# Kernel tuning notes

Measured on AMD Instinct MI355X. Metric: run time of the kernel, lower is better.

Reference implementation:

```python
import jax, jax.numpy as jnp
import numpy as np

B, T, K, U, C, M, H = 64, 600, 10, 64, 54, 20, 512
OUT = 1 + 6 * M        # 121
IN1 = 3 + C            # 57  -> rnn_cell1 input
IN2 = 3 + C + H        # 569 -> rnn_cell2 input
BIAS = 0.0
EPS = 1e-20


def setup_inputs() -> dict:
    key = jax.random.key(0)
    ks = jax.random.split(key, 20)
    p = lambda k, shape: (jax.random.normal(k, shape, dtype=jnp.float32) * 0.05)
    return {
        "x": jax.random.normal(ks[0], (B, T, 3), dtype=jnp.float32),
        "y": jax.random.uniform(ks[1], (B, T, 3), dtype=jnp.float32),
        "c_vec": jax.random.uniform(ks[2], (B, U, C), dtype=jnp.float32),
        "W_ih1": p(ks[3], (4 * H, IN1)), "W_hh1": p(ks[4], (4 * H, H)),
        "b_ih1": p(ks[5], (4 * H,)),     "b_hh1": p(ks[6], (4 * H,)),
        "W_ih2": p(ks[7], (4 * H, IN2)), "W_hh2": p(ks[8], (4 * H, H)),
        "b_ih2": p(ks[9], (4 * H,)),     "b_hh2": p(ks[10], (4 * H,)),
        "W_k": p(ks[11], (3 * K, H)),    "b_k": p(ks[12], (3 * K,)),
        "W_o": p(ks[13], (OUT, H)),      "b_o": p(ks[14], (OUT,)),
    }


def _lstm_cell(xin, h, c, Wih, Whh, bih, bhh):
    g = xin @ Wih.T + h @ Whh.T + bih + bhh          # [B, 4H]
    i, f, gg, o = jnp.split(g, 4, axis=1)            # PyTorch LSTMCell gate order
    c = jax.nn.sigmoid(f) * c + jax.nn.sigmoid(i) * jnp.tanh(gg)
    h = jax.nn.sigmoid(o) * jnp.tanh(c)
    return h, c


def _forward(x, y, c_vec, W_ih1, W_hh1, b_ih1, b_hh1, W_ih2, W_hh2, b_ih2, b_hh2,
             W_k, b_k, W_o, b_o):
    u = jnp.arange(U, dtype=jnp.float32)[None, None, :]   # [1,1,U]
    zB = jnp.zeros((B, H), dtype=x.dtype)

    def step(carry, xt):
        h1, c1, h2, c2, w, kappa = carry
        h1, c1 = _lstm_cell(jnp.concatenate([xt, w], 1), h1, c1, W_ih1, W_hh1, b_ih1, b_hh1)
        kg = h1 @ W_k.T + b_k                               # [B, 3K]
        a_hat, be_hat, ka_hat = jnp.split(kg, 3, axis=1)
        alpha = jnp.exp(a_hat)[:, :, None]                  # [B,K,1]
        beta = jnp.exp(be_hat)[:, :, None]
        kappa = kappa + jnp.exp(ka_hat)[:, :, None]
        phi = jnp.sum(jnp.exp(-beta * (kappa - u) ** 2) * alpha, axis=1)  # [B,U]
        w = jnp.einsum('bu,buc->bc', phi, c_vec)            # [B,C]
        h2, c2 = _lstm_cell(jnp.concatenate([xt, h1, w], 1), h2, c2, W_ih2, W_hh2, b_ih2, b_hh2)
        return (h1, c1, h2, c2, w, kappa), h2

    init = (zB, zB, zB, zB, jnp.zeros((B, C), x.dtype), jnp.zeros((B, K, 1), x.dtype))
    _, h2_seq = jax.lax.scan(step, init, jnp.transpose(x, (1, 0, 2)))   # [T,B,H]
    h2_seq = jnp.transpose(h2_seq, (1, 0, 2)).reshape(-1, H)            # [B*T,H]
    outputs = h2_seq @ W_o.T + b_o                                      # [B*T,OUT]

    y1, y2, s = jnp.moveaxis(y.reshape(-1, 3), 1, 0)                    # each [B*T]
    e = jax.nn.sigmoid(-outputs[:, 0])                                  # 1/(1+exp(o0))
    pi_hat, mu1, mu2, s1_hat, s2_hat, rho_hat = jnp.split(outputs[:, 1:], 6, axis=1)
    pi = jax.nn.softmax(pi_hat, axis=1)
    sigma1 = jnp.exp(s1_hat - BIAS)
    sigma2 = jnp.exp(s2_hat - BIAS)
    rho = jnp.tanh(rho_hat)
    d1 = (y1[:, None] - mu1) / sigma1
    d2 = (y2[:, None] - mu2) / sigma2
    z = d1 ** 2 + d2 ** 2 - 2.0 * rho * d1 * d2
    one_m_r2 = 1.0 - rho ** 2
    gauss = jnp.exp(-z / (2.0 * one_m_r2)) / (2.0 * np.pi * sigma1 * sigma2 * jnp.sqrt(one_m_r2))
    loss_g = jnp.sum(-jnp.log(jnp.sum(pi * gauss, axis=1) + EPS))
    loss_b = jnp.sum(-jnp.log((e + EPS) * s + (1.0 - e + EPS) * (1.0 - s)))
    return (loss_g + loss_b) / (B * T)


def reference(x, y, c_vec, W_ih1, W_hh1, b_ih1, b_hh1, W_ih2, W_hh2, b_ih2, b_hh2,
              W_k, b_k, W_o, b_o):
    return _forward(x, y, c_vec, W_ih1, W_hh1, b_ih1, b_hh1, W_ih2, W_hh2,
                    b_ih2, b_hh2, W_k, b_k, W_o, b_o)
```

## Files before the change

### kernel.cpp

```cpp
#include <hip/hip_runtime.h>
#include <math.h>

typedef _Float16 f16;
typedef _Float16 f16x8 __attribute__((ext_vector_type(8)));
typedef float f32x4 __attribute__((ext_vector_type(4)));
union HU { f16 h; unsigned short u; };

#define NT 512
#define NG1 16
#define G2B 16
#define NG2 16
#define PRB 32
#define ATB 33
#define NBLK 97
#define ABE 69632
#define ABEH 69632
#define OUTG_OFF 69632
#define LOSS_OFF 86016
#define FLAG_OFF 86144
#define W2OFF_F 86400
#define W1OFF_F 1200512
#define WPOFF_F 1790336
#define G2PER 139264
#define G1PER 73728
#define DYN_LDS 136704
#define G1LW 520
#define G2LW 1032
#define PRLW 520

__device__ __forceinline__ f16x8 cld16(const void* p) {
  f16x8 r;
  asm volatile("global_load_dwordx4 %0, %1, off sc0 sc1" : "=v"(r) : "v"(p) : "memory");
  return r;
}
__device__ __forceinline__ unsigned long long ald64(const void* p) {
  return __hip_atomic_load((const unsigned long long*)p, __ATOMIC_RELAXED, __HIP_MEMORY_SCOPE_AGENT);
}
__device__ __forceinline__ unsigned ald32(const void* p) {
  return __hip_atomic_load((const unsigned*)p, __ATOMIC_RELAXED, __HIP_MEMORY_SCOPE_AGENT);
}
__device__ __forceinline__ void cst32(void* p, unsigned v) {
  asm volatile("global_store_dword %0, %1, off sc0 sc1" :: "v"(p), "v"(v) : "memory");
}
__device__ __forceinline__ void cst128h(void* p, f16x8 v) {
  asm volatile("global_store_dwordx4 %0, %1, off sc0 sc1" :: "v"(p), "v"(v) : "memory");
}
__device__ __forceinline__ void cst128f(void* p, f32x4 v) {
  asm volatile("global_store_dwordx4 %0, %1, off sc0 sc1" :: "v"(p), "v"(v) : "memory");
}
#define VMWAIT() do { asm volatile("s_waitcnt vmcnt(0)" ::: "memory"); \
                      __builtin_amdgcn_sched_barrier(0); } while (0)

__device__ __forceinline__ float sigm(float v){ return 1.f/(1.f+expf(-v)); }

__device__ __forceinline__ void gbar(unsigned* flags, unsigned target) {
  VMWAIT();
  __syncthreads();
  if (threadIdx.x == 0) cst32(flags + blockIdx.x, target);
  if (threadIdx.x < 64) {
    bool ok;
    do {
      unsigned lo = target, hi = target;
      if (threadIdx.x < 49) {
        unsigned long long v = ald64(flags + threadIdx.x * 2);
        lo = (unsigned)v; hi = (unsigned)(v >> 32);
      }
      ok = (lo >= target) && (hi >= target);
    } while (!__all(ok));
  }
  __syncthreads();
}

__device__ __forceinline__ void wspin(const unsigned* wflags, unsigned target) {
  int lane = threadIdx.x & 63;
  bool ok;
  do {
    unsigned lo = target, hi = target;
    if (lane < 32) {
      unsigned long long v = ald64(wflags + lane * 2);
      lo = (unsigned)v; hi = (unsigned)(v >> 32);
    }
    ok = (lo >= target) && (hi >= target);
  } while (!__all(ok));
}

__device__ __forceinline__ float mix_loss(const float* so, const float* yl, int t, int m) {
  float y1 = yl[t*3+0], y2 = yl[t*3+1], ys = yl[t*3+2];
  float ph = (m < 20) ? so[1+m] : -1e30f;
  float mx = ph;
  #pragma unroll
  for (int d = 16; d >= 1; d >>= 1) mx = fmaxf(mx, __shfl_xor(mx, d));
  float pe = (m < 20) ? expf(ph - mx) : 0.f;
  float ps = pe;
  #pragma unroll
  for (int d = 16; d >= 1; d >>= 1) ps += __shfl_xor(ps, d);
  float contrib = 0.f;
  if (m < 20) {
    float mu1 = so[21+m], mu2 = so[41+m];
    float s1 = expf(so[61+m]), s2 = expf(so[81+m]);
    float rh = tanhf(so[101+m]);
    float d1 = (y1-mu1)/s1, d2 = (y2-mu2)/s2;
    float omr = 1.f - rh*rh;
    float z = d1*d1 + d2*d2 - 2.f*rh*d1*d2;
    float ga = expf(-z/(2.f*omr)) / (6.283185307179586f * s1 * s2 * sqrtf(omr));
    contrib = (pe/ps)*ga;
  }
  float gs = contrib;
  #pragma unroll
  for (int d = 16; d >= 1; d >>= 1) gs += __shfl_xor(gs, d);
  float lg = -logf(gs + 1e-20f);
  float e = 1.f/(1.f + expf(so[0]));
  float lb = -logf((e + 1e-20f)*ys + (1.f - e + 1e-20f)*(1.f - ys));
  return lg + lb;
}

__global__ __launch_bounds__(256) void k_init(float* ws,
    const float* __restrict__ Wih1, const float* __restrict__ Whh1,
    const float* __restrict__ Wih2, const float* __restrict__ Whh2,
    const float* __restrict__ Wo)
{
  unsigned* w0 = (unsigned*)ws;
  unsigned* fl = (unsigned*)ws + FLAG_OFF;
  int idx = blockIdx.x*256 + threadIdx.x;
  int str = gridDim.x*256;
  for (int e = idx; e < ABE; e += str) w0[e] = 0u;
  for (int e = idx; e < 2*8192 + 64; e += str) w0[OUTG_OFF + e] = 0u;
  if (idx < 256) fl[idx] = (idx < NBLK) ? 0u : (idx < 128 ? 0x7fffffffu : 0u);

  f16* w2p = (f16*)(ws + W2OFF_F);
  f16* w1p = (f16*)(ws + W1OFF_F);
  f16* wpp = (f16*)(ws + WPOFF_F);
  const int G2T = 16*G2PER, G1T = 16*G1PER, PPT = 65536;
  for (int e = idx; e < G2T; e += str) {
    int bi = e / G2PER, r0 = e - bi*G2PER;
    int sub = r0 & 7, frag = r0 >> 3;
    int l = frag & 63, t = frag >> 6;
    int nt = t & 7, j = t >> 3;
    int n = nt*16 + (l & 15);
    int R = (n & 3)*512 + bi*32 + (n >> 2);
    int k = j*32 + ((l >> 4) << 3) + sub;
    float v = 0.f;
    if (k >= 4 && k < 58)        v = Wih2[R*569 + 515 + (k-4)];
    else if (k >= 58 && k < 61)  v = Wih2[R*569 + (k-58)];
    else if (k >= 64 && k < 576) v = Wih2[R*569 + 3 + (k-64)];
    else if (k >= 576)           v = Whh2[R*512 + (k-576)];
    w2p[e] = (f16)v;
  }
  for (int e = idx; e < G1T; e += str) {
    int bi = e / G1PER, r0 = e - bi*G1PER;
    int sub = r0 & 7, frag = r0 >> 3;
    int l = frag & 63, t = frag >> 6;
    int nt = t & 7, j = t >> 3;
    int n = nt*16 + (l & 15);
    int R = (n & 3)*512 + bi*32 + (n >> 2);
    int k = j*32 + ((l >> 4) << 3) + sub;
    float v = 0.f;
    if (k < 3)                   v = Wih1[R*57 + k];
    else if (k >= 4 && k < 58)   v = Wih1[R*57 + 3 + (k-4)];
    else if (k >= 64 && k < 576) v = Whh1[R*512 + (k-64)];
    w1p[e] = (f16)v;
  }
  for (int e = idx; e < PPT; e += str) {
    int sub = e & 7, frag = e >> 3;
    int l = frag & 63, t = frag >> 6;
    int nt = t & 7, j = t >> 3;
    int o = nt*16 + (l & 15);
    int k = j*32 + ((l >> 4) << 3) + sub;
    wpp[e] = (o < 121) ? (f16)Wo[o*512 + k] : (f16)0.f;
  }
}

__global__ __launch_bounds__(NT, 1) void kmain(
    const float* __restrict__ x, const float* __restrict__ y, const float* __restrict__ cvec,
    const float* __restrict__ Wih1, const float* __restrict__ Whh1,
    const float* __restrict__ bih1, const float* __restrict__ bhh1,
    const float* __restrict__ Wih2, const float* __restrict__ Whh2,
    const float* __restrict__ bih2, const float* __restrict__ bhh2,
    const float* __restrict__ Wk, const float* __restrict__ bk,
    const float* __restrict__ Wo, const float* __restrict__ bo,
    float* __restrict__ out, float* __restrict__ ws)
{
  extern __shared__ char dsm[];
  const int blk = blockIdx.x, tid = threadIdx.x;
  const int wv = tid >> 6, l = tid & 63;
  const int q = l & 3;

  f16* AB = (f16*)ws;
  float* outg  = ws + OUTG_OFF;
  float* lossg = ws + LOSS_OFF;
  unsigned* flags  = (unsigned*)ws + FLAG_OFF;
  unsigned* wflags = flags + 128;
  const f16* __restrict__ w2pA = (const f16*)(ws + W2OFF_F);
  const f16* __restrict__ w1pA = (const f16*)(ws + W1OFF_F);
  const f16* __restrict__ wppA = (const f16*)(ws + WPOFF_F);

  f32x4 acc[4];
  float cst[16];
  float bi0 = 0.f, bpr = 0.f, lreg = 0.f;
  #pragma unroll
  for (int z = 0; z < 16; ++z) cst[z] = 0.f;

  if (blk < NG1) {
    int n = wv*16 + (l & 15);
    int R = (n & 3)*512 + blk*32 + (n >> 2);
    bi0 = bih1[R] + bhh1[R];
  } else if (blk < G2B + NG2) {
    const int g2i = blk - G2B;
    int n = wv*16 + (l & 15);
    int R = (n & 3)*512 + g2i*32 + (n >> 2);
    bi0 = bih2[R] + bhh2[R];
  } else if (blk == PRB) {
    int o = wv*16 + (l & 15);
    bpr = (o < 121) ? bo[o] : 0.f;
  } else {
    const int b = blk - ATB;
    f16*   wk  = (f16*)dsm;
    float* cv  = (float*)(dsm + 31200);
    float* xl  = (float*)(dsm + 45024);
    float* yl  = (float*)(dsm + 52224);
    for (int e = tid; e < 30*512; e += NT) { int j = e >> 9, k = e & 511; wk[j*520 + k] = (f16)Wk[e]; }
    for (int e = tid; e < 3456; e += NT) cv[e] = cvec[b*3456 + e];
    for (int e = tid; e < 1800; e += NT) { xl[e] = x[b*1800+e]; yl[e] = y[b*1800+e]; }
    float* kap = (float*)(dsm + 61152);
    if (tid < 10) kap[tid] = 0.f;
    __syncthreads();
    if (tid == 0) {
      HU h0, h1u, h2u;
      h0.h = (f16)xl[0]; h1u.h = (f16)xl[1]; h2u.h = (f16)xl[2];
      cst32((unsigned*)AB + (b*1088 >> 1),       (unsigned)h0.u | ((unsigned)h1u.u << 16));
      cst32((unsigned*)AB + ((b*1088 + 2) >> 1), (unsigned)h2u.u);
    }
  }

  gbar(flags, 1);

  for (int t = 0; t <= 602; ++t) {
    const f16* __restrict__ Acur = AB + (t & 1)*ABEH;
    f16* __restrict__ Anxt = AB + ((t & 1)^1)*ABEH;
    unsigned* AcurW = (unsigned*)Acur;

    if (blk < NG1) {
      if (t <= 599) {
        const f16* __restrict__ wp = w1pA + blk*G1PER;
        f16* plds = (f16*)dsm;
        f16* htr  = (f16*)(dsm + 66560);
        {
          f16x8 tb[8];
          #pragma unroll
          for (int it = 0; it < 8; ++it) {
            int flat = tid + it*512;
            tb[it] = cld16(Acur + (flat >> 6)*1088 + 64 + (flat & 63)*8);
          }
          VMWAIT();
          #pragma unroll
          for (int it = 0; it < 8; ++it) {
            int flat = tid + it*512;
            *(f16x8*)&plds[(flat >> 6)*G1LW + (flat & 63)*8] = tb[it];
          }
        }
        __syncthreads();
        #pragma unroll
        for (int z = 0; z < 4; ++z) acc[z] = (f32x4){0,0,0,0};
        const int kb = (l >> 4)*8;
        #pragma unroll 8
        for (int j = 2; j < 18; ++j) {
          f16x8 bfr = *(const f16x8*)(wp + ((j*8 + wv)*64 + l)*8);
          #pragma unroll
          for (int mt = 0; mt < 4; ++mt) {
            f16x8 af = *(const f16x8*)&plds[((l&15) + 16*mt)*G1LW + (j*32 - 64) + kb];
            acc[mt] = __builtin_amdgcn_mfma_f32_16x16x32_f16(af, bfr, acc[mt], 0,0,0);
          }
        }
        wspin(wflags, (unsigned)t);
        {
          f16x8 a01[4][2];
          #pragma unroll
          for (int mt = 0; mt < 4; ++mt)
            #pragma unroll
            for (int jd = 0; jd < 2; ++jd)
              a01[mt][jd] = cld16(Acur + ((l&15) + 16*mt)*1088 + jd*32 + kb);
          VMWAIT();
          #pragma unroll
          for (int jd = 0; jd < 2; ++jd) {
            f16x8 bfr = *(const f16x8*)(wp + ((jd*8 + wv)*64 + l)*8);
            #pragma unroll
            for (int mt = 0; mt < 4; ++mt)
              acc[mt] = __builtin_amdgcn_mfma_f32_16x16x32_f16(a01[mt][jd], bfr, acc[mt], 0,0,0);
          }
        }
        {
          int dloc = wv*4 + ((l & 15) >> 2);
          #pragma unroll
          for (int mt = 0; mt < 4; ++mt)
            #pragma unroll
            for (int r = 0; r < 4; ++r) {
              float xme = acc[mt][r] + bi0;
              float a1 = __shfl_xor(xme, 1), a2 = __shfl_xor(xme, 2), a3 = __shfl_xor(a1, 2);
              float gi = q==0?xme: q==1?a1 : q==2?a2 : a3;
              float gf = q==0?a1 : q==1?xme: q==2?a3 : a2;
              float gg = q==0?a2 : q==1?a3 : q==2?xme: a1;
              float go = q==0?a3 : q==1?a2 : q==2?a1 : xme;
              float c = cst[mt*4 + r];
              c = sigm(gf)*c + sigm(gi)*tanhf(gg);
              cst[mt*4 + r] = c;
              float h = sigm(go)*tanhf(c);
              if (q == 0) htr[(mt*16 + (l>>4)*4 + r)*32 + dloc] = (f16)h;
            }
        }
        __syncthreads();
        if (tid < 256) {
          int m = tid >> 2, qq = tid & 3;
          f16x8 hv = *(const f16x8*)&htr[m*32 + qq*8];
          cst128h(Anxt + m*1088 + 64 + blk*32 + qq*8, hv);
        }
      }
    } else if (blk < G2B + NG2) {
      if (t >= 1 && t <= 600) {
        const int g2i = blk - G2B;
        const f16* __restrict__ wp = w2pA + g2i*G2PER;
        f16* plds = (f16*)dsm;
        f16* htr  = (f16*)(dsm + 132096);
        {
          f16x8 tb[16];
          #pragma unroll
          for (int it = 0; it < 16; ++it) {
            int flat = tid + it*512;
            tb[it] = cld16(Acur + (flat >> 7)*1088 + 64 + (flat & 127)*8);
          }
          VMWAIT();
          #pragma unroll
          for (int it = 0; it < 16; ++it) {
            int flat = tid + it*512;
            *(f16x8*)&plds[(flat >> 7)*G2LW + (flat & 127)*8] = tb[it];
          }
        }
        __syncthreads();
        #pragma unroll
        for (int z = 0; z < 4; ++z) acc[z] = (f32x4){0,0,0,0};
        const int kb = (l >> 4)*8;
        #pragma unroll 8
        for (int j = 2; j < 34; ++j) {
          f16x8 bfr = *(const f16x8*)(wp + ((j*8 + wv)*64 + l)*8);
          #pragma unroll
          for (int mt = 0; mt < 4; ++mt) {
            f16x8 af = *(const f16x8*)&plds[((l&15) + 16*mt)*G2LW + (j*32 - 64) + kb];
            acc[mt] = __builtin_amdgcn_mfma_f32_16x16x32_f16(af, bfr, acc[mt], 0,0,0);
          }
        }
        wspin(wflags, (unsigned)t);
        {
          f16x8 a01[4][2];
          #pragma unroll
          for (int mt = 0; mt < 4; ++mt)
            #pragma unroll
            for (int jd = 0; jd < 2; ++jd)
              a01[mt][jd] = cld16(Acur + ((l&15) + 16*mt)*1088 + jd*32 + kb);
          VMWAIT();
          #pragma unroll
          for (int jd = 0; jd < 2; ++jd) {
            f16x8 bfr = *(const f16x8*)(wp + ((jd*8 + wv)*64 + l)*8);
            #pragma unroll
            for (int mt = 0; mt < 4; ++mt)
              acc[mt] = __builtin_amdgcn_mfma_f32_16x16x32_f16(a01[mt][jd], bfr, acc[mt], 0,0,0);
          }
        }
        {
          int dloc = wv*4 + ((l & 15) >> 2);
          #pragma unroll
          for (int mt = 0; mt < 4; ++mt)
            #pragma unroll
            for (int r = 0; r < 4; ++r) {
              float xme = acc[mt][r] + bi0;
              float a1 = __shfl_xor(xme, 1), a2 = __shfl_xor(xme, 2), a3 = __shfl_xor(a1, 2);
              float gi = q==0?xme: q==1?a1 : q==2?a2 : a3;
              float gf = q==0?a1 : q==1?xme: q==2?a3 : a2;
              float gg = q==0?a2 : q==1?a3 : q==2?xme: a1;
              float go = q==0?a3 : q==1?a2 : q==2?a1 : xme;
              float c = cst[mt*4 + r];
              c = sigm(gf)*c + sigm(gi)*tanhf(gg);
              cst[mt*4 + r] = c;
              float h = sigm(go)*tanhf(c);
              if (q == 0) htr[(mt*16 + (l>>4)*4 + r)*32 + dloc] = (f16)h;
            }
        }
        __syncthreads();
        if (tid < 256) {
          int m = tid >> 2, qq = tid & 3;
          f16x8 hv = *(const f16x8*)&htr[m*32 + qq*8];
          cst128h(Anxt + m*1088 + 576 + g2i*32 + qq*8, hv);
        }
      }
    } else if (blk == PRB) {
      if (t >= 2 && t <= 601) {
        f16* plds = (f16*)dsm;
        float* otr = (float*)(dsm + 66560);
        float* outp = outg + (t & 1)*8192;
        {
          f16x8 tb[8];
          #pragma unroll
          for (int it = 0; it < 8; ++it) {
            int flat = tid + it*512;
            tb[it] = cld16(Acur + (flat >> 6)*1088 + 576 + (flat & 63)*8);
          }
          VMWAIT();
          #pragma unroll
          for (int it = 0; it < 8; ++it) {
            int flat = tid + it*512;
            *(f16x8*)&plds[(flat >> 6)*PRLW + (flat & 63)*8] = tb[it];
          }
        }
        __syncthreads();
        #pragma unroll
        for (int z = 0; z < 4; ++z) acc[z] = (f32x4){0,0,0,0};
        const int kb = (l >> 4)*8;
        #pragma unroll 8
        for (int j = 0; j < 16; ++j) {
          f16x8 bfr = *(const f16x8*)(wppA + ((j*8 + wv)*64 + l)*8);
          #pragma unroll
          for (int mt = 0; mt < 4; ++mt) {
            f16x8 af = *(const f16x8*)&plds[((l&15) + 16*mt)*PRLW + j*32 + kb];
            acc[mt] = __builtin_amdgcn_mfma_f32_16x16x32_f16(af, bfr, acc[mt], 0,0,0);
          }
        }
        { int o = wv*16 + (l & 15);
          #pragma unroll
          for (int mt = 0; mt < 4; ++mt)
            #pragma unroll
            for (int r = 0; r < 4; ++r)
              otr[(mt*16 + (l>>4)*4 + r)*128 + o] = acc[mt][r] + bpr;
        }
        __syncthreads();
        #pragma unroll
        for (int it = 0; it < 4; ++it) {
          int flat = tid + it*512;
          int m = flat >> 5, o4 = flat & 31;
          f32x4 v4 = *(const f32x4*)&otr[m*128 + o4*4];
          cst128f(outp + m*128 + o4*4, v4);
        }
      }
    } else {
      const int b = blk - ATB;
      f16*   wk   = (f16*)dsm;
      float* cv   = (float*)(dsm + 31200);
      float* xl   = (float*)(dsm + 45024);
      float* yl   = (float*)(dsm + 52224);
      f16*   h1h  = (f16*)(dsm + 59424);
      float* so   = (float*)(dsm + 60448);
      float* skg  = (float*)(dsm + 60944);
      float* sal  = (float*)(dsm + 61072);
      float* sbe  = (float*)(dsm + 61112);
      float* kap  = (float*)(dsm + 61152);
      float* sphi = (float*)(dsm + 61192);
      float* wtmp = (float*)(dsm + 61448);
      if (t >= 1 && t <= 600) {
        const int s = t - 1;
        if (tid < 64) {
          f16x8 hv = cld16(Acur + b*1088 + 64 + tid*8);
          VMWAIT();
          *(f16x8*)&h1h[tid*8] = hv;
        }
        __syncthreads();
        {
          int j = tid >> 4, ksv = tid & 15;
          float a = 0.f;
          if (j < 30) {
            const f16* wr = &wk[j*520 + ksv*32];
            const f16* hr = &h1h[ksv*32];
            #pragma unroll
            for (int c = 0; c < 4; ++c) {
              f16x8 qv = *(const f16x8*)(wr + c*8);
              f16x8 hv = *(const f16x8*)(hr + c*8);
              #pragma unroll
              for (int e = 0; e < 8; ++e) a += (float)qv[e] * (float)hv[e];
            }
          }
          a += __shfl_xor(a, 1); a += __shfl_xor(a, 2);
          a += __shfl_xor(a, 4); a += __shfl_xor(a, 8);
          if (j < 30 && ksv == 0) skg[j] = a + bk[j];
        }
        __syncthreads();
        if (tid < 10) {
          sal[tid] = expf(skg[tid]);
          sbe[tid] = expf(skg[10+tid]);
          kap[tid] += expf(skg[20+tid]);
        }
        __syncthreads();
        if (tid < 64) {
          float u = (float)tid, ph = 0.f;
          #pragma unroll
          for (int k2 = 0; k2 < 10; ++k2) {
            float d = kap[k2] - u;
            ph += sal[k2]*expf(-sbe[k2]*d*d);
          }
          sphi[tid] = ph;
        }
        __syncthreads();
        if (tid < 54) {
          float wvv = 0.f;
          #pragma unroll 8
          for (int u = 0; u < 64; ++u) wvv += sphi[u]*cv[u*54 + tid];
          wtmp[tid] = wvv;
        }
        __syncthreads();
        if (tid < 27) {
          HU a, bu; a.h = (f16)wtmp[2*tid]; bu.h = (f16)wtmp[2*tid+1];
          cst32(AcurW + ((b*1088 + 4 + 2*tid) >> 1), (unsigned)a.u | ((unsigned)bu.u << 16));
        } else if (tid == 27) {
          HU a, bu; a.h = (f16)xl[s*3+0]; bu.h = (f16)xl[s*3+1];
          cst32(AcurW + ((b*1088 + 58) >> 1), (unsigned)a.u | ((unsigned)bu.u << 16));
        } else if (tid == 28) {
          HU a; a.h = (f16)xl[s*3+2];
          cst32(AcurW + ((b*1088 + 60) >> 1), (unsigned)a.u);
        } else if (tid == 29 && s <= 598) {
          HU a, bu; a.h = (f16)xl[(s+1)*3+0]; bu.h = (f16)xl[(s+1)*3+1];
          cst32(AcurW + ((b*1088) >> 1), (unsigned)a.u | ((unsigned)bu.u << 16));
        } else if (tid == 30 && s <= 598) {
          HU a; a.h = (f16)xl[(s+1)*3+2];
          cst32(AcurW + ((b*1088 + 2) >> 1), (unsigned)a.u);
        }
        VMWAIT();
        __syncthreads();
        if (tid == 0) cst32(wflags + b, (unsigned)t);
      }
      if (t >= 3) {
        if (tid < 121) {
          unsigned uu = ald32((unsigned*)(outg + ((t & 1)^1)*8192) + b*128 + tid);
          float v; __builtin_memcpy(&v, &uu, 4);
          so[tid] = v;
        }
        __syncthreads();
        if (tid < 32) {
          float v = mix_loss(so, yl, t-3, tid);
          if (tid == 0) lreg += v;
        }
      }
    }
    gbar(flags, 2 + t);
  }

  if (blk >= ATB && tid == 0) {
    unsigned uu; __builtin_memcpy(&uu, &lreg, 4);
    cst32((unsigned*)lossg + (blk - ATB), uu);
  }
  gbar(flags, 606);
  if (blk == ATB && tid < 64) {
    unsigned uu = ald32((unsigned*)lossg + tid);
    float v; __builtin_memcpy(&v, &uu, 4);
    #pragma unroll
    for (int d = 32; d >= 1; d >>= 1) v += __shfl_xor(v, d);
    if (tid == 0) out[0] = v / 38400.f;
  }
}

extern "C" void kernel_launch(void* const* d_in, const int* in_sizes, int n_in,
                              void* d_out, int out_size, void* d_ws, size_t ws_size,
                              hipStream_t stream)
{
  (void)in_sizes; (void)n_in; (void)out_size; (void)ws_size;
  const float* x    = (const float*)d_in[0];
  const float* y    = (const float*)d_in[1];
  const float* cvec = (const float*)d_in[2];
  const float* Wih1 = (const float*)d_in[3];
  const float* Whh1 = (const float*)d_in[4];
  const float* bih1 = (const float*)d_in[5];
  const float* bhh1 = (const float*)d_in[6];
  const float* Wih2 = (const float*)d_in[7];
  const float* Whh2 = (const float*)d_in[8];
  const float* bih2 = (const float*)d_in[9];
  const float* bhh2 = (const float*)d_in[10];
  const float* Wk   = (const float*)d_in[11];
  const float* bk   = (const float*)d_in[12];
  const float* Wo   = (const float*)d_in[13];
  const float* bo   = (const float*)d_in[14];
  float* out = (float*)d_out;
  float* wsf = (float*)d_ws;

  hipFuncSetAttribute((const void*)kmain, hipFuncAttributeMaxDynamicSharedMemorySize, DYN_LDS);

  k_init<<<256, 256, 0, stream>>>(wsf, Wih1, Whh1, Wih2, Whh2, Wo);

  void* args[] = {
    (void*)&x, (void*)&y, (void*)&cvec,
    (void*)&Wih1, (void*)&Whh1, (void*)&bih1, (void*)&bhh1,
    (void*)&Wih2, (void*)&Whh2, (void*)&bih2, (void*)&bhh2,
    (void*)&Wk, (void*)&bk, (void*)&Wo, (void*)&bo,
    (void*)&out, (void*)&wsf
  };
  hipLaunchCooperativeKernel((void*)kmain, dim3(NBLK), dim3(NT), args, DYN_LDS, stream);
}
```

Before: 12.80 ms.

## Restructure per-step pipeline so attention waits on h1 flags within the step

Attention blocks now compute the window vector for step t in the same global-barrier interval. They spin on new per-block h1 flags written by the LSTM1 blocks, then write w into the next buffer. LSTM1 no longer waits on attention flags mid-GEMM and loads the full input row (x, w and h1) in one pass. Barrier flags are padded to separate 64-byte slots to avoid false sharing during polling. This changes the cross-stage schedule and dependency chain, with some risk of lengthening the critical path within each step.

```diff
diff --git a/kernel.cpp b/kernel.cpp
--- a/kernel.cpp
+++ b/kernel.cpp
@@ -18,13 +18,14 @@
 #define OUTG_OFF 69632
 #define LOSS_OFF 86016
 #define FLAG_OFF 86144
-#define W2OFF_F 86400
-#define W1OFF_F 1200512
-#define WPOFF_F 1790336
+#define HFLG_OFF 87744
+#define W2OFF_F 88064
+#define W1OFF_F 1202176
+#define WPOFF_F 1792000
 #define G2PER 139264
 #define G1PER 73728
 #define DYN_LDS 136704
-#define G1LW 520
+#define G1LW 584
 #define G2LW 1032
 #define PRLW 520
 
@@ -33,9 +34,6 @@
   asm volatile("global_load_dwordx4 %0, %1, off sc0 sc1" : "=v"(r) : "v"(p) : "memory");
   return r;
 }
-__device__ __forceinline__ unsigned long long ald64(const void* p) {
-  return __hip_atomic_load((const unsigned long long*)p, __ATOMIC_RELAXED, __HIP_MEMORY_SCOPE_AGENT);
-}
 __device__ __forceinline__ unsigned ald32(const void* p) {
   return __hip_atomic_load((const unsigned*)p, __ATOMIC_RELAXED, __HIP_MEMORY_SCOPE_AGENT);
 }
@@ -56,32 +54,17 @@
 __device__ __forceinline__ void gbar(unsigned* flags, unsigned target) {
   VMWAIT();
   __syncthreads();
-  if (threadIdx.x == 0) cst32(flags + blockIdx.x, target);
+  if (threadIdx.x == 0) cst32(flags + blockIdx.x * 16, target);
   if (threadIdx.x < 64) {
+    int lane = threadIdx.x;
     bool ok;
     do {
-      unsigned lo = target, hi = target;
-      if (threadIdx.x < 49) {
-        unsigned long long v = ald64(flags + threadIdx.x * 2);
-        lo = (unsigned)v; hi = (unsigned)(v >> 32);
-      }
-      ok = (lo >= target) && (hi >= target);
+      unsigned v0 = ald32(flags + lane * 16);
+      unsigned v1 = (lane < 33) ? ald32(flags + (64 + lane) * 16) : target;
+      ok = (v0 >= target) && (v1 >= target);
     } while (!__all(ok));
   }
   __syncthreads();
-}
-
-__device__ __forceinline__ void wspin(const unsigned* wflags, unsigned target) {
-  int lane = threadIdx.x & 63;
-  bool ok;
-  do {
-    unsigned lo = target, hi = target;
-    if (lane < 32) {
-      unsigned long long v = ald64(wflags + lane * 2);
-      lo = (unsigned)v; hi = (unsigned)(v >> 32);
-    }
-    ok = (lo >= target) && (hi >= target);
-  } while (!__all(ok));
 }
 
 __device__ __forceinline__ float mix_loss(const float* so, const float* yl, int t, int m) {
@@ -120,12 +103,11 @@
     const float* __restrict__ Wo)
 {
   unsigned* w0 = (unsigned*)ws;
-  unsigned* fl = (unsigned*)ws + FLAG_OFF;
   int idx = blockIdx.x*256 + threadIdx.x;
   int str = gridDim.x*256;
   for (int e = idx; e < ABE; e += str) w0[e] = 0u;
   for (int e = idx; e < 2*8192 + 64; e += str) w0[OUTG_OFF + e] = 0u;
-  if (idx < 256) fl[idx] = (idx < NBLK) ? 0u : (idx < 128 ? 0x7fffffffu : 0u);
+  for (int e = idx; e < HFLG_OFF + 256 - FLAG_OFF; e += str) w0[FLAG_OFF + e] = 0u;
 
   f16* w2p = (f16*)(ws + W2OFF_F);
   f16* w1p = (f16*)(ws + W1OFF_F);
@@ -189,7 +171,7 @@
   float* outg  = ws + OUTG_OFF;
   float* lossg = ws + LOSS_OFF;
   unsigned* flags  = (unsigned*)ws + FLAG_OFF;
-  unsigned* wflags = flags + 128;
+  unsigned* hflags = (unsigned*)ws + HFLG_OFF;
   const f16* __restrict__ w2pA = (const f16*)(ws + W2OFF_F);
   const f16* __restrict__ w1pA = (const f16*)(ws + W1OFF_F);
   const f16* __restrict__ wppA = (const f16*)(ws + WPOFF_F);
@@ -237,55 +219,40 @@
   for (int t = 0; t <= 602; ++t) {
     const f16* __restrict__ Acur = AB + (t & 1)*ABEH;
     f16* __restrict__ Anxt = AB + ((t & 1)^1)*ABEH;
-    unsigned* AcurW = (unsigned*)Acur;
+    unsigned* AnxtW = (unsigned*)Anxt;
 
     if (blk < NG1) {
       if (t <= 599) {
         const f16* __restrict__ wp = w1pA + blk*G1PER;
         f16* plds = (f16*)dsm;
-        f16* htr  = (f16*)(dsm + 66560);
-        {
-          f16x8 tb[8];
-          #pragma unroll
-          for (int it = 0; it < 8; ++it) {
-            int flat = tid + it*512;
-            tb[it] = cld16(Acur + (flat >> 6)*1088 + 64 + (flat & 63)*8);
+        f16* htr  = (f16*)(dsm + 74752);
+        {
+          f16x8 tb[9];
+          #pragma unroll
+          for (int it = 0; it < 9; ++it) {
+            int flat = it*512 + tid;
+            int row = flat / 72, c8 = flat - row*72;
+            tb[it] = cld16(Acur + row*1088 + c8*8);
           }
           VMWAIT();
           #pragma unroll
-          for (int it = 0; it < 8; ++it) {
-            int flat = tid + it*512;
-            *(f16x8*)&plds[(flat >> 6)*G1LW + (flat & 63)*8] = tb[it];
+          for (int it = 0; it < 9; ++it) {
+            int flat = it*512 + tid;
+            int row = flat / 72, c8 = flat - row*72;
+            *(f16x8*)&plds[row*G1LW + c8*8] = tb[it];
           }
         }
         __syncthreads();
         #pragma unroll
         for (int z = 0; z < 4; ++z) acc[z] = (f32x4){0,0,0,0};
         const int kb = (l >> 4)*8;
-        #pragma unroll 8
-        for (int j = 2; j < 18; ++j) {
+        #pragma unroll 6
+        for (int j = 0; j < 18; ++j) {
           f16x8 bfr = *(const f16x8*)(wp + ((j*8 + wv)*64 + l)*8);
           #pragma unroll
           for (int mt = 0; mt < 4; ++mt) {
-            f16x8 af = *(const f16x8*)&plds[((l&15) + 16*mt)*G1LW + (j*32 - 64) + kb];
+            f16x8 af = *(const f16x8*)&plds[((l&15) + 16*mt)*G1LW + j*32 + kb];
             acc[mt] = __builtin_amdgcn_mfma_f32_16x16x32_f16(af, bfr, acc[mt], 0,0,0);
-          }
-        }
-        wspin(wflags, (unsigned)t);
-        {
-          f16x8 a01[4][2];
-          #pragma unroll
-          for (int mt = 0; mt < 4; ++mt)
-            #pragma unroll
-            for (int jd = 0; jd < 2; ++jd)
-              a01[mt][jd] = cld16(Acur + ((l&15) + 16*mt)*1088 + jd*32 + kb);
-          VMWAIT();
-          #pragma unroll
-          for (int jd = 0; jd < 2; ++jd) {
-            f16x8 bfr = *(const f16x8*)(wp + ((jd*8 + wv)*64 + l)*8);
-            #pragma unroll
-            for (int mt = 0; mt < 4; ++mt)
-              acc[mt] = __builtin_amdgcn_mfma_f32_16x16x32_f16(a01[mt][jd], bfr, acc[mt], 0,0,0);
           }
         }
         {
@@ -313,6 +280,9 @@
           f16x8 hv = *(const f16x8*)&htr[m*32 + qq*8];
           cst128h(Anxt + m*1088 + 64 + blk*32 + qq*8, hv);
         }
+        VMWAIT();
+        __syncthreads();
+        if (tid == 0) cst32(hflags + blk*16, (unsigned)(t + 1));
       }
     } else if (blk < G2B + NG2) {
       if (t >= 1 && t <= 600) {
@@ -347,7 +317,6 @@
             acc[mt] = __builtin_amdgcn_mfma_f32_16x16x32_f16(af, bfr, acc[mt], 0,0,0);
           }
         }
-        wspin(wflags, (unsigned)t);
         {
           f16x8 a01[4][2];
           #pragma unroll
@@ -452,10 +421,31 @@
       float* kap  = (float*)(dsm + 61152);
       float* sphi = (float*)(dsm + 61192);
       float* wtmp = (float*)(dsm + 61448);
-      if (t >= 1 && t <= 600) {
-        const int s = t - 1;
+      if (t >= 3) {
+        if (tid < 121) {
+          unsigned uu = ald32((unsigned*)(outg + ((t & 1)^1)*8192) + b*128 + tid);
+          float v; __builtin_memcpy(&v, &uu, 4);
+          so[tid] = v;
+        }
+        __syncthreads();
+        if (tid < 32) {
+          float v = mix_loss(so, yl, t-3, tid);
+          if (tid == 0) lreg += v;
+        }
+        __syncthreads();
+      }
+      if (t <= 599) {
+        const int s = t;
         if (tid < 64) {
-          f16x8 hv = cld16(Acur + b*1088 + 64 + tid*8);
+          bool ok;
+          do {
+            unsigned v = (tid < 16) ? ald32(hflags + tid*16) : (unsigned)(t+1);
+            ok = v >= (unsigned)(t+1);
+          } while (!__all(ok));
+        }
+        __syncthreads();
+        if (tid < 64) {
+          f16x8 hv = cld16(Anxt + b*1088 + 64 + tid*8);
           VMWAIT();
           *(f16x8*)&h1h[tid*8] = hv;
         }
@@ -504,34 +494,19 @@
         __syncthreads();
         if (tid < 27) {
           HU a, bu; a.h = (f16)wtmp[2*tid]; bu.h = (f16)wtmp[2*tid+1];
-          cst32(AcurW + ((b*1088 + 4 + 2*tid) >> 1), (unsigned)a.u | ((unsigned)bu.u << 16));
+          cst32(AnxtW + ((b*1088 + 4 + 2*tid) >> 1), (unsigned)a.u | ((unsigned)bu.u << 16));
         } else if (tid == 27) {
           HU a, bu; a.h = (f16)xl[s*3+0]; bu.h = (f16)xl[s*3+1];
-          cst32(AcurW + ((b*1088 + 58) >> 1), (unsigned)a.u | ((unsigned)bu.u << 16));
+          cst32(AnxtW + ((b*1088 + 58) >> 1), (unsigned)a.u | ((unsigned)bu.u << 16));
         } else if (tid == 28) {
           HU a; a.h = (f16)xl[s*3+2];
-          cst32(AcurW + ((b*1088 + 60) >> 1), (unsigned)a.u);
+          cst32(AnxtW + ((b*1088 + 60) >> 1), (unsigned)a.u);
         } else if (tid == 29 && s <= 598) {
           HU a, bu; a.h = (f16)xl[(s+1)*3+0]; bu.h = (f16)xl[(s+1)*3+1];
-          cst32(AcurW + ((b*1088) >> 1), (unsigned)a.u | ((unsigned)bu.u << 16));
+          cst32(AnxtW + ((b*1088) >> 1), (unsigned)a.u | ((unsigned)bu.u << 16));
         } else if (tid == 30 && s <= 598) {
           HU a; a.h = (f16)xl[(s+1)*3+2];
-          cst32(AcurW + ((b*1088 + 2) >> 1), (unsigned)a.u);
-        }
-        VMWAIT();
-        __syncthreads();
-        if (tid == 0) cst32(wflags + b, (unsigned)t);
-      }
-      if (t >= 3) {
-        if (tid < 121) {
-          unsigned uu = ald32((unsigned*)(outg + ((t & 1)^1)*8192) + b*128 + tid);
-          float v; __builtin_memcpy(&v, &uu, 4);
-          so[tid] = v;
-        }
-        __syncthreads();
-        if (tid < 32) {
-          float v = mix_loss(so, yl, t-3, tid);
-          if (tid == 0) lreg += v;
+          cst32(AnxtW + ((b*1088 + 2) >> 1), (unsigned)a.u);
         }
       }
     }
@@ -542,7 +517,7 @@
     unsigned uu; __builtin_memcpy(&uu, &lreg, 4);
     cst32((unsigned*)lossg + (blk - ATB), uu);
   }
-  gbar(flags, 606);
+  gbar(flags, 610);
   if (blk == ATB && tid < 64) {
     unsigned uu = ald32((unsigned*)lossg + tid);
     float v; __builtin_memcpy(&v, &uu, 4);
```

After: 11.27 ms. 1.14x faster.
